# Optimization experiments

Measured on AMD Instinct MI355X. Metric: run time of the kernel, lower is better.

Reference implementation:

```python
import jax, jax.numpy as jnp
import numpy as np

N = 100000   # nodes
DEG = 4      # fixed out-degree (>2 so every node survives the c>2 mask)
E = N * DEG  # edges
IN = 128
H = 256


def _lin_params(key, fan_out, fan_in, bias=True):
    k1, k2 = jax.random.split(key)
    W = 0.05 * jax.random.normal(k1, (fan_out, fan_in), jnp.float32)
    if bias:
        b = 0.05 * jax.random.normal(k2, (fan_out,), jnp.float32)
        return W, b
    return W


def setup_inputs() -> dict:
    key = jax.random.key(0)
    ks = jax.random.split(key, 12)
    x = jax.random.normal(ks[0], (N, IN), jnp.float32)
    # every node has exactly DEG outgoing edges -> out-degree 4 > 2 for all nodes
    src = jnp.repeat(jnp.arange(N, dtype=jnp.int32), DEG)
    dst = jax.random.randint(ks[1], (E,), 0, N, dtype=jnp.int32)
    edge_index = jnp.stack([src, dst])  # [2, E]
    batch = jnp.zeros((N,), jnp.int32)
    Wr0, br0 = _lin_params(ks[2], H, IN)
    Ws0 = _lin_params(ks[3], H, IN, bias=False)
    Wr1, br1 = _lin_params(ks[4], H, H)
    Ws1 = _lin_params(ks[5], H, H, bias=False)
    Wr2, br2 = _lin_params(ks[6], H, H)
    Ws2 = _lin_params(ks[7], H, H, bias=False)
    Wsp1, bsp1 = _lin_params(ks[8], 1, H)
    Wsp2, bsp2 = _lin_params(ks[9], 1, H)
    Wl, bl = _lin_params(ks[10], 1, 2)
    return dict(x=x, edge_index=edge_index, batch=batch,
                Wr0=Wr0, br0=br0, Ws0=Ws0,
                Wr1=Wr1, br1=br1, Ws1=Ws1,
                Wr2=Wr2, br2=br2, Ws2=Ws2,
                Wsp1=Wsp1, bsp1=bsp1, Wsp2=Wsp2, bsp2=bsp2,
                Wl=Wl, bl=bl)


def reference(x, edge_index, batch, Wr0, br0, Ws0, Wr1, br1, Ws1,
              Wr2, br2, Ws2, Wsp1, bsp1, Wsp2, bsp2, Wl, bl):
    src, dst = edge_index[0], edge_index[1]

    def gconv(h, Wr, br, Ws):
        # PyG GraphConv(aggr='add'): out_i = W_rel @ sum_{j->i} h_j + b + W_root @ h_i
        agg = jax.ops.segment_sum(h[src], dst, num_segments=N)
        return jax.nn.relu(agg @ Wr.T + br + h @ Ws.T)

    h = gconv(x, Wr0, br0, Ws0)
    h = gconv(h, Wr1, br1, Ws1)
    h = gconv(h, Wr2, br2, Ws2)

    # unique(edge_index[0], counts) ; keep source nodes with out-degree > 2
    deg = jax.ops.segment_sum(jnp.ones((E,), h.dtype), src, num_segments=N)
    sel = jnp.nonzero(deg > 2, size=N, fill_value=0)[0]  # all N nodes by construction
    xs = h[sel].reshape(-1, 2 * H)  # pair consecutive nodes
    x1, x2 = xs[:, :H], xs[:, H:]
    out = jnp.concatenate([jax.nn.relu(x1 @ Wsp1.T + bsp1),
                           jax.nn.relu(x2 @ Wsp2.T + bsp2)], axis=1)
    y = jax.nn.sigmoid(out @ Wl.T + bl)  # split=True branch
    return y, xs, x1, x2
```

## Files before the change

kernel.cpp:

```cpp
#include <hip/hip_runtime.h>
#include <hip/hip_bf16.h>
#include <math.h>

#define NNODES 100000
#define NEDGES 400000
#define INDIM  128
#define HDIM   256
#define MAXDEG 32

#define BM 64
#define BN 256
#define BK 64
#define MTILES 1563

typedef __attribute__((ext_vector_type(8))) short short8;
typedef __attribute__((ext_vector_type(8))) unsigned short ushort8v;
typedef __attribute__((ext_vector_type(4))) float f32x4;

__device__ __forceinline__ float bf2f(unsigned short u) {
    union { unsigned int i; float f; } v; v.i = ((unsigned int)u) << 16; return v.f;
}
__device__ __forceinline__ unsigned short f2bf(float f) {
    union { float f; unsigned int i; } v; v.f = f;
    unsigned int r = v.i + 0x7fffu + ((v.i >> 16) & 1u);
    return (unsigned short)(r >> 16);
}

__device__ __forceinline__ void async_load16(const void* g, void* l) {
    __builtin_amdgcn_global_load_lds(
        (const __attribute__((address_space(1))) unsigned int*)g,
        (__attribute__((address_space(3))) unsigned int*)l,
        16, 0, 0);
}

#define XB_BLOCKS 12500
#define W0_BLOCKS 256
#define W1_BLOCKS 512
#define EL_BLOCKS 1563
#define PREP_BLOCKS (XB_BLOCKS + W0_BLOCKS + 2 * W1_BLOCKS + EL_BLOCKS)

__global__ void prep_kernel(const float* __restrict__ x, unsigned short* __restrict__ xb,
                            const float* __restrict__ Wr0, const float* __restrict__ Ws0,
                            unsigned short* __restrict__ B0,
                            const float* __restrict__ Wr1, const float* __restrict__ Ws1,
                            unsigned short* __restrict__ B1,
                            const float* __restrict__ Wr2, const float* __restrict__ Ws2,
                            unsigned short* __restrict__ B2,
                            const int* __restrict__ ei, int* __restrict__ cnt,
                            int* __restrict__ elist) {
    int b = blockIdx.x;
    if (b < XB_BLOCKS) {
        int i = b * 256 + threadIdx.x;
        float4 v = ((const float4*)x)[i];
        ushort4 o; o.x = f2bf(v.x); o.y = f2bf(v.y); o.z = f2bf(v.z); o.w = f2bf(v.w);
        ((ushort4*)xb)[i] = o;
        return;
    }
    b -= XB_BLOCKS;
    if (b < W0_BLOCKS + 2 * W1_BLOCKS) {
        const float *Wr, *Ws; unsigned short* B; int K;
        if (b < W0_BLOCKS)               { Wr = Wr0; Ws = Ws0; B = B0; K = INDIM; }
        else if (b < W0_BLOCKS + W1_BLOCKS) { Wr = Wr1; Ws = Ws1; B = B1; K = HDIM; b -= W0_BLOCKS; }
        else                              { Wr = Wr2; Ws = Ws2; B = B2; K = HDIM; b -= W0_BLOCKS + W1_BLOCKS; }
        int idx = b * 256 + threadIdx.x;
        int n = idx / (2 * K);
        int k = idx - n * 2 * K;
        float v = (k < K) ? Wr[n * K + k] : Ws[n * K + (k - K)];
        B[idx] = f2bf(v);
        return;
    }
    b -= W0_BLOCKS + 2 * W1_BLOCKS;
    int e = b * 256 + threadIdx.x;
    if (e < NEDGES) {
        int d = ei[NEDGES + e];
        int s = ei[e];
        int pos = atomicAdd(&cnt[d], 1);
        if (pos < MAXDEG) elist[d * MAXDEG + pos] = s;
    }
}

__global__ void gather_bf16_128(const unsigned short* __restrict__ h, const int* __restrict__ cnt,
                                const int* __restrict__ elist, unsigned short* __restrict__ agg) {
    int wid  = (blockIdx.x * blockDim.x + threadIdx.x) >> 6;
    int lane = threadIdx.x & 63;
    if (wid >= NNODES) return;
    int c = cnt[wid]; if (c > MAXDEG) c = MAXDEG;
    const int4* el4 = (const int4*)(elist + wid * MAXDEG);
    float a0 = 0.f, a1 = 0.f;
    for (int j0 = 0; j0 < c; j0 += 4) {
        int4 e = el4[j0 >> 2];
        int rem = c - j0;
        ushort2 v0 = {0,0}, v1 = {0,0}, v2 = {0,0}, v3 = {0,0};
        v0 = ((const ushort2*)(h + (size_t)e.x * INDIM))[lane];
        if (rem > 1) v1 = ((const ushort2*)(h + (size_t)e.y * INDIM))[lane];
        if (rem > 2) v2 = ((const ushort2*)(h + (size_t)e.z * INDIM))[lane];
        if (rem > 3) v3 = ((const ushort2*)(h + (size_t)e.w * INDIM))[lane];
        a0 += bf2f(v0.x) + bf2f(v1.x) + bf2f(v2.x) + bf2f(v3.x);
        a1 += bf2f(v0.y) + bf2f(v1.y) + bf2f(v2.y) + bf2f(v3.y);
    }
    ushort2 o; o.x = f2bf(a0); o.y = f2bf(a1);
    ((ushort2*)(agg + (size_t)wid * INDIM))[lane] = o;
}

__global__ void gather_bf16_256(const unsigned short* __restrict__ h, const int* __restrict__ cnt,
                                const int* __restrict__ elist, unsigned short* __restrict__ agg) {
    int wid  = (blockIdx.x * blockDim.x + threadIdx.x) >> 6;
    int lane = threadIdx.x & 63;
    if (wid >= NNODES) return;
    int c = cnt[wid]; if (c > MAXDEG) c = MAXDEG;
    const int4* el4 = (const int4*)(elist + wid * MAXDEG);
    float a0 = 0.f, a1 = 0.f, a2 = 0.f, a3 = 0.f;
    for (int j0 = 0; j0 < c; j0 += 4) {
        int4 e = el4[j0 >> 2];
        int rem = c - j0;
        ushort4 v0 = {0,0,0,0}, v1 = {0,0,0,0}, v2 = {0,0,0,0}, v3 = {0,0,0,0};
        v0 = ((const ushort4*)(h + (size_t)e.x * HDIM))[lane];
        if (rem > 1) v1 = ((const ushort4*)(h + (size_t)e.y * HDIM))[lane];
        if (rem > 2) v2 = ((const ushort4*)(h + (size_t)e.z * HDIM))[lane];
        if (rem > 3) v3 = ((const ushort4*)(h + (size_t)e.w * HDIM))[lane];
        a0 += bf2f(v0.x) + bf2f(v1.x) + bf2f(v2.x) + bf2f(v3.x);
        a1 += bf2f(v0.y) + bf2f(v1.y) + bf2f(v2.y) + bf2f(v3.y);
        a2 += bf2f(v0.z) + bf2f(v1.z) + bf2f(v2.z) + bf2f(v3.z);
        a3 += bf2f(v0.w) + bf2f(v1.w) + bf2f(v2.w) + bf2f(v3.w);
    }
    ushort4 o; o.x = f2bf(a0); o.y = f2bf(a1); o.z = f2bf(a2); o.w = f2bf(a3);
    ((ushort4*)(agg + (size_t)wid * HDIM))[lane] = o;
}

template<int MODE>
__global__ __launch_bounds__(256)
void gemm_kernel(const unsigned short* __restrict__ A1, const unsigned short* __restrict__ A2,
                 int K, const unsigned short* __restrict__ B, const float* __restrict__ bias,
                 unsigned short* __restrict__ hout,
                 float* __restrict__ xs, float* __restrict__ x1o, float* __restrict__ x2o,
                 const float* __restrict__ Wsp1, const float* __restrict__ Wsp2,
                 float* __restrict__ spart) {
    __shared__ __align__(16) unsigned char smem[(BM * BK + BN * BK) * 2];
    unsigned short* Ash = (unsigned short*)smem;
    unsigned short* Bsh = Ash + BM * BK;

    const int tid  = threadIdx.x;
    const int lane = tid & 63;
    const int wn   = tid >> 6;
    const int m0   = blockIdx.x * BM;
    const int Ktot = 2 * K;

    f32x4 acc[4][4];
    for (int i = 0; i < 4; i++)
        for (int j = 0; j < 4; j++)
            acc[i][j] = (f32x4){0.f, 0.f, 0.f, 0.f};

    for (int k0 = 0; k0 < Ktot; k0 += BK) {
        const unsigned short* Abase; int koff;
        if (k0 < K) { Abase = A1; koff = k0; } else { Abase = A2; koff = k0 - K; }

        #pragma unroll
        for (int it = 0; it < 2; it++) {
            int idx = it * 256 + tid;
            int row = idx >> 3, seg = idx & 7;
            int gseg = seg ^ (row & 7);
            int grow = m0 + row; if (grow >= NNODES) grow = NNODES - 1;
            async_load16(Abase + (size_t)grow * K + koff + gseg * 8, &Ash[idx * 8]);
        }
        #pragma unroll
        for (int it = 0; it < 8; it++) {
            int idx = it * 256 + tid;
            int row = idx >> 3, seg = idx & 7;
            int gseg = seg ^ (row & 7);
            async_load16(B + (size_t)row * Ktot + k0 + gseg * 8, &Bsh[idx * 8]);
        }
        __syncthreads();

        #pragma unroll
        for (int half = 0; half < 2; half++) {
            short8 af[4], bfr[4];
            #pragma unroll
            for (int mt = 0; mt < 4; mt++) {
                int ml  = mt * 16 + (lane & 15);
                int seg = half * 4 + (lane >> 4);
                int ps  = seg ^ (ml & 7);
                af[mt] = *(const short8*)&Ash[ml * BK + ps * 8];
            }
            #pragma unroll
            for (int nt = 0; nt < 4; nt++) {
                int nl  = wn * 64 + nt * 16 + (lane & 15);
                int seg = half * 4 + (lane >> 4);
                int ps  = seg ^ (nl & 7);
                bfr[nt] = *(const short8*)&Bsh[nl * BK + ps * 8];
            }
            #pragma unroll
            for (int mt = 0; mt < 4; mt++)
                #pragma unroll
                for (int nt = 0; nt < 4; nt++)
                    acc[mt][nt] = __builtin_amdgcn_mfma_f32_16x16x32_bf16(
                        af[mt], bfr[nt], acc[mt][nt], 0, 0, 0);
        }
        __syncthreads();
    }

    float* bounce = (float*)smem;
    float* wb = bounce + wn * (16 * 68);
    const int q    = lane & 3;
    const int rrow = lane >> 2;

    #pragma unroll
    for (int mt = 0; mt < 4; mt++) {
        __syncthreads();
        #pragma unroll
        for (int nt = 0; nt < 4; nt++)
            #pragma unroll
            for (int rr = 0; rr < 4; rr++)
                wb[((lane >> 4) * 4 + rr) * 68 + nt * 16 + (lane & 15)] = acc[mt][nt][rr];
        __syncthreads();

        int grow = m0 + mt * 16 + rrow;
        int gc   = wn * 64 + q * 16;
        float4 v[4];
        #pragma unroll
        for (int s = 0; s < 4; s++)
            v[s] = ((const float4*)(wb + rrow * 68 + q * 16))[s];

        if (grow < NNODES) {
            const float4* bv = (const float4*)(bias + gc);
            #pragma unroll
            for (int s = 0; s < 4; s++) {
                float4 b4 = bv[s];
                v[s].x = fmaxf(v[s].x + b4.x, 0.f);
                v[s].y = fmaxf(v[s].y + b4.y, 0.f);
                v[s].z = fmaxf(v[s].z + b4.z, 0.f);
                v[s].w = fmaxf(v[s].w + b4.w, 0.f);
            }
            if (MODE == 0) {
                ushort8v o0, o1;
                o0[0]=f2bf(v[0].x); o0[1]=f2bf(v[0].y); o0[2]=f2bf(v[0].z); o0[3]=f2bf(v[0].w);
                o0[4]=f2bf(v[1].x); o0[5]=f2bf(v[1].y); o0[6]=f2bf(v[1].z); o0[7]=f2bf(v[1].w);
                o1[0]=f2bf(v[2].x); o1[1]=f2bf(v[2].y); o1[2]=f2bf(v[2].z); o1[3]=f2bf(v[2].w);
                o1[4]=f2bf(v[3].x); o1[5]=f2bf(v[3].y); o1[6]=f2bf(v[3].z); o1[7]=f2bf(v[3].w);
                ushort8v* dst = (ushort8v*)(hout + (size_t)grow * HDIM + gc);
                dst[0] = o0; dst[1] = o1;
            } else {
                float4* xsp = (float4*)(xs + (size_t)grow * HDIM + gc);
                #pragma unroll
                for (int s = 0; s < 4; s++) xsp[s] = v[s];
                float* xo = (grow & 1) ? x2o : x1o;
                float4* xop = (float4*)(xo + (size_t)(grow >> 1) * HDIM + gc);
                #pragma unroll
                for (int s = 0; s < 4; s++) xop[s] = v[s];
                const float* wsp = (grow & 1) ? Wsp2 : Wsp1;
                const float4* wv = (const float4*)(wsp + gc);
                float p = 0.f;
                #pragma unroll
                for (int s = 0; s < 4; s++) {
                    float4 w4 = wv[s];
                    p += v[s].x * w4.x + v[s].y * w4.y + v[s].z * w4.z + v[s].w * w4.w;
                }
                p += __shfl_xor(p, 1);
                p += __shfl_xor(p, 2);
                if (q == 0) atomicAdd(&spart[grow], p);
            }
        }
    }
}

__global__ void finalize_kernel(const float* __restrict__ spart, const float* __restrict__ bsp1,
                                const float* __restrict__ bsp2, const float* __restrict__ Wl,
                                const float* __restrict__ bl, float* __restrict__ y) {
    int p = blockIdx.x * 256 + threadIdx.x;
    if (p < NNODES / 2) {
        float s1 = spart[2 * p]     + bsp1[0]; s1 = s1 > 0.f ? s1 : 0.f;
        float s2 = spart[2 * p + 1] + bsp2[0]; s2 = s2 > 0.f ? s2 : 0.f;
        float t = s1 * Wl[0] + s2 * Wl[1] + bl[0];
        y[p] = 1.f / (1.f + expf(-t));
    }
}

extern "C" void kernel_launch(void* const* d_in, const int* in_sizes, int n_in,
                              void* d_out, int out_size, void* d_ws, size_t ws_size,
                              hipStream_t stream) {
    const float* x    = (const float*)d_in[0];
    const int*   ei   = (const int*)d_in[1];
    const float* Wr0  = (const float*)d_in[3];
    const float* br0  = (const float*)d_in[4];
    const float* Ws0  = (const float*)d_in[5];
    const float* Wr1  = (const float*)d_in[6];
    const float* br1  = (const float*)d_in[7];
    const float* Ws1  = (const float*)d_in[8];
    const float* Wr2  = (const float*)d_in[9];
    const float* br2  = (const float*)d_in[10];
    const float* Ws2  = (const float*)d_in[11];
    const float* Wsp1 = (const float*)d_in[12];
    const float* bsp1 = (const float*)d_in[13];
    const float* Wsp2 = (const float*)d_in[14];
    const float* bsp2 = (const float*)d_in[15];
    const float* Wl   = (const float*)d_in[16];
    const float* bl   = (const float*)d_in[17];

    char* ws = (char*)d_ws;
    size_t off = 0;
    auto alloc = [&](size_t bytes) -> void* {
        void* p = ws + off;
        off += (bytes + 255) & ~(size_t)255;
        return p;
    };
    int*            cnt   = (int*)alloc((size_t)NNODES * 4);
    float*          spart = (float*)alloc((size_t)NNODES * 4);
    size_t zero_bytes = off;
    int*            elist = (int*)alloc((size_t)NNODES * MAXDEG * 4);
    unsigned short* xb    = (unsigned short*)alloc((size_t)NNODES * INDIM * 2);
    unsigned short* aggb  = (unsigned short*)alloc((size_t)NNODES * HDIM * 2);
    unsigned short* hA    = (unsigned short*)alloc((size_t)NNODES * HDIM * 2);
    unsigned short* hB    = (unsigned short*)alloc((size_t)NNODES * HDIM * 2);
    unsigned short* B0    = (unsigned short*)alloc((size_t)HDIM * 2 * INDIM * 2);
    unsigned short* B1    = (unsigned short*)alloc((size_t)HDIM * 2 * HDIM * 2);
    unsigned short* B2    = (unsigned short*)alloc((size_t)HDIM * 2 * HDIM * 2);

    float* y  = (float*)d_out;
    float* xs = y + 50000;
    float* x1 = xs + (size_t)50000 * 512;
    float* x2 = x1 + (size_t)50000 * 256;

    hipMemsetAsync(ws, 0, zero_bytes, stream);
    prep_kernel<<<PREP_BLOCKS, 256, 0, stream>>>(x, xb, Wr0, Ws0, B0, Wr1, Ws1, B1,
                                                 Wr2, Ws2, B2, ei, cnt, elist);

    int gather_blocks = (NNODES * 64 + 255) / 256;

    gather_bf16_128<<<gather_blocks, 256, 0, stream>>>(xb, cnt, elist, aggb);
    gemm_kernel<0><<<MTILES, 256, 0, stream>>>(aggb, xb, INDIM, B0, br0, hA,
                                               nullptr, nullptr, nullptr,
                                               nullptr, nullptr, nullptr);
    gather_bf16_256<<<gather_blocks, 256, 0, stream>>>(hA, cnt, elist, aggb);
    gemm_kernel<0><<<MTILES, 256, 0, stream>>>(aggb, hA, HDIM, B1, br1, hB,
                                               nullptr, nullptr, nullptr,
                                               nullptr, nullptr, nullptr);
    gather_bf16_256<<<gather_blocks, 256, 0, stream>>>(hB, cnt, elist, aggb);
    gemm_kernel<1><<<MTILES, 256, 0, stream>>>(aggb, hB, HDIM, B2, br2, nullptr,
                                               xs, x1, x2, Wsp1, Wsp2, spart);
    finalize_kernel<<<(NNODES / 2 + 255) / 256, 256, 0, stream>>>(
        spart, bsp1, bsp2, Wl, bl, y);
}
```

Baseline: 609.3 us.

## Fuse neighbor gather-aggregation into GEMM kernel via shared-memory aggregate tile

The separate gather kernels are removed. Each GEMM block now gathers and sums neighbor rows for its 64 nodes directly into a 32KB LDS tile (swizzled), then runs the MFMA loop reading the aggregated half of A from LDS and the self half from global. This is meant to remove the global write and re-read of the aggregate buffer and two kernel launches per layer. In exchange, LDS grows to 64KB per block, which lowers occupancy, and the gather latency is no longer overlapped across separate wide kernels.

```diff
diff --git a/kernel.cpp b/kernel.cpp
--- a/kernel.cpp
+++ b/kernel.cpp
@@ -79,111 +79,174 @@
     }
 }
 
-__global__ void gather_bf16_128(const unsigned short* __restrict__ h, const int* __restrict__ cnt,
-                                const int* __restrict__ elist, unsigned short* __restrict__ agg) {
-    int wid  = (blockIdx.x * blockDim.x + threadIdx.x) >> 6;
-    int lane = threadIdx.x & 63;
-    if (wid >= NNODES) return;
-    int c = cnt[wid]; if (c > MAXDEG) c = MAXDEG;
-    const int4* el4 = (const int4*)(elist + wid * MAXDEG);
-    float a0 = 0.f, a1 = 0.f;
-    for (int j0 = 0; j0 < c; j0 += 4) {
-        int4 e = el4[j0 >> 2];
-        int rem = c - j0;
-        ushort2 v0 = {0,0}, v1 = {0,0}, v2 = {0,0}, v3 = {0,0};
-        v0 = ((const ushort2*)(h + (size_t)e.x * INDIM))[lane];
-        if (rem > 1) v1 = ((const ushort2*)(h + (size_t)e.y * INDIM))[lane];
-        if (rem > 2) v2 = ((const ushort2*)(h + (size_t)e.z * INDIM))[lane];
-        if (rem > 3) v3 = ((const ushort2*)(h + (size_t)e.w * INDIM))[lane];
-        a0 += bf2f(v0.x) + bf2f(v1.x) + bf2f(v2.x) + bf2f(v3.x);
-        a1 += bf2f(v0.y) + bf2f(v1.y) + bf2f(v2.y) + bf2f(v3.y);
-    }
-    ushort2 o; o.x = f2bf(a0); o.y = f2bf(a1);
-    ((ushort2*)(agg + (size_t)wid * INDIM))[lane] = o;
-}
-
-__global__ void gather_bf16_256(const unsigned short* __restrict__ h, const int* __restrict__ cnt,
-                                const int* __restrict__ elist, unsigned short* __restrict__ agg) {
-    int wid  = (blockIdx.x * blockDim.x + threadIdx.x) >> 6;
-    int lane = threadIdx.x & 63;
-    if (wid >= NNODES) return;
-    int c = cnt[wid]; if (c > MAXDEG) c = MAXDEG;
-    const int4* el4 = (const int4*)(elist + wid * MAXDEG);
-    float a0 = 0.f, a1 = 0.f, a2 = 0.f, a3 = 0.f;
-    for (int j0 = 0; j0 < c; j0 += 4) {
-        int4 e = el4[j0 >> 2];
-        int rem = c - j0;
-        ushort4 v0 = {0,0,0,0}, v1 = {0,0,0,0}, v2 = {0,0,0,0}, v3 = {0,0,0,0};
-        v0 = ((const ushort4*)(h + (size_t)e.x * HDIM))[lane];
-        if (rem > 1) v1 = ((const ushort4*)(h + (size_t)e.y * HDIM))[lane];
-        if (rem > 2) v2 = ((const ushort4*)(h + (size_t)e.z * HDIM))[lane];
-        if (rem > 3) v3 = ((const ushort4*)(h + (size_t)e.w * HDIM))[lane];
-        a0 += bf2f(v0.x) + bf2f(v1.x) + bf2f(v2.x) + bf2f(v3.x);
-        a1 += bf2f(v0.y) + bf2f(v1.y) + bf2f(v2.y) + bf2f(v3.y);
-        a2 += bf2f(v0.z) + bf2f(v1.z) + bf2f(v2.z) + bf2f(v3.z);
-        a3 += bf2f(v0.w) + bf2f(v1.w) + bf2f(v2.w) + bf2f(v3.w);
-    }
-    ushort4 o; o.x = f2bf(a0); o.y = f2bf(a1); o.z = f2bf(a2); o.w = f2bf(a3);
-    ((ushort4*)(agg + (size_t)wid * HDIM))[lane] = o;
-}
-
 template<int MODE>
 __global__ __launch_bounds__(256)
-void gemm_kernel(const unsigned short* __restrict__ A1, const unsigned short* __restrict__ A2,
+void fused_gconv(const unsigned short* __restrict__ h,
+                 const int* __restrict__ cnt, const int* __restrict__ elist,
                  int K, const unsigned short* __restrict__ B, const float* __restrict__ bias,
                  unsigned short* __restrict__ hout,
                  float* __restrict__ xs, float* __restrict__ x1o, float* __restrict__ x2o,
                  const float* __restrict__ Wsp1, const float* __restrict__ Wsp2,
                  float* __restrict__ spart) {
-    __shared__ __align__(16) unsigned char smem[(BM * BK + BN * BK) * 2];
-    unsigned short* Ash = (unsigned short*)smem;
-    unsigned short* Bsh = Ash + BM * BK;
+    __shared__ __align__(16) unsigned char smem[65536];
+    unsigned short* Agg = (unsigned short*)smem;
+    unsigned short* Bsh = (unsigned short*)(smem + 32768);
 
     const int tid  = threadIdx.x;
     const int lane = tid & 63;
-    const int wn   = tid >> 6;
+    const int wv   = tid >> 6;
     const int m0   = blockIdx.x * BM;
     const int Ktot = 2 * K;
 
+    const int lane31 = lane & 31;
+    const int hw     = lane >> 5;
+    int pn = m0 + wv * 16 + (lane >> 2);
+    if (pn >= NNODES) pn = NNODES - 1;
+    const int4 elv = ((const int4*)(elist + (size_t)pn * MAXDEG))[lane & 3];
+    int cnode = m0 + wv * 16 + (lane & 15);
+    if (cnode >= NNODES) cnode = NNODES - 1;
+    const int cv = cnt[cnode];
+
+    #pragma unroll
+    for (int it = 0; it < 8; it++) {
+        int idx = it * 256 + tid;
+        int row = idx >> 3, seg = idx & 7;
+        int gseg = seg ^ (row & 7);
+        async_load16(B + (size_t)row * Ktot + gseg * 8, &Bsh[idx * 8]);
+    }
+
+    if (K == 256) {
+        for (int rd = 0; rd < 8; rd++) {
+            const int iw = rd * 2 + hw;
+            int cA = __shfl(cv, rd * 2);
+            int cB = __shfl(cv, rd * 2 + 1);
+            if (cA > MAXDEG) cA = MAXDEG;
+            if (cB > MAXDEG) cB = MAXDEG;
+            const int c    = hw ? cB : cA;
+            const int cmax = cA > cB ? cA : cB;
+            int node = m0 + wv * 16 + iw;
+            if (node >= NNODES) node = NNODES - 1;
+            float a[8];
+            #pragma unroll
+            for (int i = 0; i < 8; i++) a[i] = 0.f;
+            for (int j0 = 0; j0 < cmax; j0 += 4) {
+                int4 e;
+                if (j0 < 16) {
+                    int src = iw * 4 + (j0 >> 2);
+                    e.x = __shfl(elv.x, src); e.y = __shfl(elv.y, src);
+                    e.z = __shfl(elv.z, src); e.w = __shfl(elv.w, src);
+                } else {
+                    e = ((const int4*)(elist + (size_t)node * MAXDEG))[j0 >> 2];
+                }
+                int rem = c - j0;
+                ushort8v v0 = {0,0,0,0,0,0,0,0}, v1 = v0, v2 = v0, v3 = v0;
+                if (rem > 0) v0 = ((const ushort8v*)(h + (size_t)e.x * 256))[lane31];
+                if (rem > 1) v1 = ((const ushort8v*)(h + (size_t)e.y * 256))[lane31];
+                if (rem > 2) v2 = ((const ushort8v*)(h + (size_t)e.z * 256))[lane31];
+                if (rem > 3) v3 = ((const ushort8v*)(h + (size_t)e.w * 256))[lane31];
+                #pragma unroll
+                for (int i = 0; i < 8; i++)
+                    a[i] += bf2f(v0[i]) + bf2f(v1[i]) + bf2f(v2[i]) + bf2f(v3[i]);
+            }
+            int r = wv * 16 + iw;
+            int sgp = (lane31 & ~7) | ((lane31 ^ r) & 7);
+            ushort8v o;
+            #pragma unroll
+            for (int i = 0; i < 8; i++) o[i] = f2bf(a[i]);
+            *(ushort8v*)&Agg[r * 256 + sgp * 8] = o;
+        }
+    } else {
+        for (int rd = 0; rd < 8; rd++) {
+            const int iw = rd * 2 + hw;
+            int cA = __shfl(cv, rd * 2);
+            int cB = __shfl(cv, rd * 2 + 1);
+            if (cA > MAXDEG) cA = MAXDEG;
+            if (cB > MAXDEG) cB = MAXDEG;
+            const int c    = hw ? cB : cA;
+            const int cmax = cA > cB ? cA : cB;
+            int node = m0 + wv * 16 + iw;
+            if (node >= NNODES) node = NNODES - 1;
+            float a0 = 0.f, a1 = 0.f, a2 = 0.f, a3 = 0.f;
+            for (int j0 = 0; j0 < cmax; j0 += 4) {
+                int4 e;
+                if (j0 < 16) {
+                    int src = iw * 4 + (j0 >> 2);
+                    e.x = __shfl(elv.x, src); e.y = __shfl(elv.y, src);
+                    e.z = __shfl(elv.z, src); e.w = __shfl(elv.w, src);
+                } else {
+                    e = ((const int4*)(elist + (size_t)node * MAXDEG))[j0 >> 2];
+                }
+                int rem = c - j0;
+                ushort4 v0 = {0,0,0,0}, v1 = {0,0,0,0}, v2 = {0,0,0,0}, v3 = {0,0,0,0};
+                if (rem > 0) v0 = ((const ushort4*)(h + (size_t)e.x * 128))[lane31];
+                if (rem > 1) v1 = ((const ushort4*)(h + (size_t)e.y * 128))[lane31];
+                if (rem > 2) v2 = ((const ushort4*)(h + (size_t)e.z * 128))[lane31];
+                if (rem > 3) v3 = ((const ushort4*)(h + (size_t)e.w * 128))[lane31];
+                a0 += bf2f(v0.x) + bf2f(v1.x) + bf2f(v2.x) + bf2f(v3.x);
+                a1 += bf2f(v0.y) + bf2f(v1.y) + bf2f(v2.y) + bf2f(v3.y);
+                a2 += bf2f(v0.z) + bf2f(v1.z) + bf2f(v2.z) + bf2f(v3.z);
+                a3 += bf2f(v0.w) + bf2f(v1.w) + bf2f(v2.w) + bf2f(v3.w);
+            }
+            int r = wv * 16 + iw;
+            int sg = lane31 >> 1;
+            int sgp = (sg & ~7) | ((sg ^ r) & 7);
+            ushort4 o; o.x = f2bf(a0); o.y = f2bf(a1); o.z = f2bf(a2); o.w = f2bf(a3);
+            *(ushort4*)&Agg[r * 128 + sgp * 8 + (lane31 & 1) * 4] = o;
+        }
+    }
+
     f32x4 acc[4][4];
+    #pragma unroll
     for (int i = 0; i < 4; i++)
+        #pragma unroll
         for (int j = 0; j < 4; j++)
             acc[i][j] = (f32x4){0.f, 0.f, 0.f, 0.f};
 
     for (int k0 = 0; k0 < Ktot; k0 += BK) {
-        const unsigned short* Abase; int koff;
-        if (k0 < K) { Abase = A1; koff = k0; } else { Abase = A2; koff = k0 - K; }
-
-        #pragma unroll
-        for (int it = 0; it < 2; it++) {
-            int idx = it * 256 + tid;
-            int row = idx >> 3, seg = idx & 7;
-            int gseg = seg ^ (row & 7);
-            int grow = m0 + row; if (grow >= NNODES) grow = NNODES - 1;
-            async_load16(Abase + (size_t)grow * K + koff + gseg * 8, &Ash[idx * 8]);
-        }
-        #pragma unroll
-        for (int it = 0; it < 8; it++) {
-            int idx = it * 256 + tid;
-            int row = idx >> 3, seg = idx & 7;
-            int gseg = seg ^ (row & 7);
-            async_load16(B + (size_t)row * Ktot + k0 + gseg * 8, &Bsh[idx * 8]);
+        if (k0 >= K) {
+            #pragma unroll
+            for (int it = 0; it < 2; it++) {
+                int idx = it * 256 + tid;
+                int row = idx >> 3, seg = idx & 7;
+                int gseg = seg ^ (row & 7);
+                int grow = m0 + row; if (grow >= NNODES) grow = NNODES - 1;
+                async_load16(h + (size_t)grow * K + (k0 - K) + gseg * 8, &Agg[idx * 8]);
+            }
+        }
+        if (k0 > 0) {
+            #pragma unroll
+            for (int it = 0; it < 8; it++) {
+                int idx = it * 256 + tid;
+                int row = idx >> 3, seg = idx & 7;
+                int gseg = seg ^ (row & 7);
+                async_load16(B + (size_t)row * Ktot + k0 + gseg * 8, &Bsh[idx * 8]);
+            }
         }
         __syncthreads();
 
         #pragma unroll
         for (int half = 0; half < 2; half++) {
             short8 af[4], bfr[4];
-            #pragma unroll
-            for (int mt = 0; mt < 4; mt++) {
-                int ml  = mt * 16 + (lane & 15);
-                int seg = half * 4 + (lane >> 4);
-                int ps  = seg ^ (ml & 7);
-                af[mt] = *(const short8*)&Ash[ml * BK + ps * 8];
+            if (k0 < K) {
+                #pragma unroll
+                for (int mt = 0; mt < 4; mt++) {
+                    int ml = mt * 16 + (lane & 15);
+                    int sg = (k0 >> 3) + half * 4 + (lane >> 4);
+                    int sgp = (sg & ~7) | ((sg ^ ml) & 7);
+                    af[mt] = *(const short8*)&Agg[ml * K + sgp * 8];
+                }
+            } else {
+                #pragma unroll
+                for (int mt = 0; mt < 4; mt++) {
+                    int ml  = mt * 16 + (lane & 15);
+                    int seg = half * 4 + (lane >> 4);
+                    int ps  = seg ^ (ml & 7);
+                    af[mt] = *(const short8*)&Agg[ml * BK + ps * 8];
+                }
             }
             #pragma unroll
             for (int nt = 0; nt < 4; nt++) {
-                int nl  = wn * 64 + nt * 16 + (lane & 15);
+                int nl  = wv * 64 + nt * 16 + (lane & 15);
                 int seg = half * 4 + (lane >> 4);
                 int ps  = seg ^ (nl & 7);
                 bfr[nt] = *(const short8*)&Bsh[nl * BK + ps * 8];
@@ -199,7 +262,7 @@
     }
 
     float* bounce = (float*)smem;
-    float* wb = bounce + wn * (16 * 68);
+    float* wb = bounce + wv * (16 * 68);
     const int q    = lane & 3;
     const int rrow = lane >> 2;
 
@@ -214,7 +277,7 @@
         __syncthreads();
 
         int grow = m0 + mt * 16 + rrow;
-        int gc   = wn * 64 + q * 16;
+        int gc   = wv * 64 + q * 16;
         float4 v[4];
         #pragma unroll
         for (int s = 0; s < 4; s++)
@@ -247,11 +310,11 @@
                 #pragma unroll
                 for (int s = 0; s < 4; s++) xop[s] = v[s];
                 const float* wsp = (grow & 1) ? Wsp2 : Wsp1;
-                const float4* wv = (const float4*)(wsp + gc);
+                const float4* wv4 = (const float4*)(wsp + gc);
                 float p = 0.f;
                 #pragma unroll
                 for (int s = 0; s < 4; s++) {
-                    float4 w4 = wv[s];
+                    float4 w4 = wv4[s];
                     p += v[s].x * w4.x + v[s].y * w4.y + v[s].z * w4.z + v[s].w * w4.w;
                 }
                 p += __shfl_xor(p, 1);
@@ -307,7 +370,6 @@
     size_t zero_bytes = off;
     int*            elist = (int*)alloc((size_t)NNODES * MAXDEG * 4);
     unsigned short* xb    = (unsigned short*)alloc((size_t)NNODES * INDIM * 2);
-    unsigned short* aggb  = (unsigned short*)alloc((size_t)NNODES * HDIM * 2);
     unsigned short* hA    = (unsigned short*)alloc((size_t)NNODES * HDIM * 2);
     unsigned short* hB    = (unsigned short*)alloc((size_t)NNODES * HDIM * 2);
     unsigned short* B0    = (unsigned short*)alloc((size_t)HDIM * 2 * INDIM * 2);
@@ -323,18 +385,13 @@
     prep_kernel<<<PREP_BLOCKS, 256, 0, stream>>>(x, xb, Wr0, Ws0, B0, Wr1, Ws1, B1,
                                                  Wr2, Ws2, B2, ei, cnt, elist);
 
-    int gather_blocks = (NNODES * 64 + 255) / 256;
-
-    gather_bf16_128<<<gather_blocks, 256, 0, stream>>>(xb, cnt, elist, aggb);
-    gemm_kernel<0><<<MTILES, 256, 0, stream>>>(aggb, xb, INDIM, B0, br0, hA,
+    fused_gconv<0><<<MTILES, 256, 0, stream>>>(xb, cnt, elist, INDIM, B0, br0, hA,
                                                nullptr, nullptr, nullptr,
                                                nullptr, nullptr, nullptr);
-    gather_bf16_256<<<gather_blocks, 256, 0, stream>>>(hA, cnt, elist, aggb);
-    gemm_kernel<0><<<MTILES, 256, 0, stream>>>(aggb, hA, HDIM, B1, br1, hB,
+    fused_gconv<0><<<MTILES, 256, 0, stream>>>(hA, cnt, elist, HDIM, B1, br1, hB,
                                                nullptr, nullptr, nullptr,
                                                nullptr, nullptr, nullptr);
-    gather_bf16_256<<<gather_blocks, 256, 0, stream>>>(hB, cnt, elist, aggb);
-    gemm_kernel<1><<<MTILES, 256, 0, stream>>>(aggb, hB, HDIM, B2, br2, nullptr,
+    fused_gconv<1><<<MTILES, 256, 0, stream>>>(hB, cnt, elist, HDIM, B2, br2, nullptr,
                                                xs, x1, x2, Wsp1, Wsp2, spart);
     finalize_kernel<<<(NNODES / 2 + 255) / 256, 256, 0, stream>>>(
         spart, bsp1, bsp2, Wl, bl, y);
```

New measurement: 603.7 us. About the same (-0.9%).
